# Kernel optimization log

Measured on AMD Instinct MI355X. Metric: run time of the kernel, lower is better.

Reference implementation:

```python
import jax, jax.numpy as jnp
import numpy as np

N_HEADS = 12


def setup_inputs() -> dict:
    key = jax.random.key(0)
    ks = jax.random.split(key, 5)
    B, T, D = 4, 2048, 768
    std = 1.0 / np.sqrt(D)
    return {
        "x": jax.random.normal(ks[0], (B, T, D), jnp.float32),
        "W_qkv": jax.random.normal(ks[1], (3 * D, D), jnp.float32) * std,
        "b_qkv": jax.random.normal(ks[2], (3 * D,), jnp.float32) * 0.02,
        "W_proj": jax.random.normal(ks[3], (D, D), jnp.float32) * std,
        "b_proj": jax.random.normal(ks[4], (D,), jnp.float32) * 0.02,
    }


def reference(x, W_qkv, b_qkv, W_proj, b_proj):
    # x: [B, T, D]; intended 3D path of the module (dropout = eval-mode identity)
    B, T, D = x.shape
    H = N_HEADS
    Dh = D // H
    scale = Dh ** -0.5
    qkv = x @ W_qkv.T + b_qkv                       # [B, T, 3D]
    qkv = qkv.reshape(B, T, 3, H, Dh)
    q = jnp.transpose(qkv[:, :, 0], (0, 2, 1, 3))    # [B, H, T, Dh]
    k = jnp.transpose(qkv[:, :, 1], (0, 2, 1, 3))
    v = jnp.transpose(qkv[:, :, 2], (0, 2, 1, 3))
    attn = jnp.einsum("bhqd,bhkd->bhqk", q, k) * scale  # [B, H, T, T]
    scores = jax.nn.softmax(attn, axis=-1)
    out = jnp.einsum("bhqk,bhkd->bhqd", scores, v)       # [B, H, T, Dh]
    out = jnp.transpose(out, (0, 2, 1, 3)).reshape(B, T, D)
    return out @ W_proj.T + b_proj
```

## Files before the change

### kernel.cpp

```cpp
#include <hip/hip_runtime.h>
#include <hip/hip_bf16.h>
#include <stdint.h>

typedef __bf16 bf16;
typedef __bf16 bf16x8 __attribute__((ext_vector_type(8)));
typedef __bf16 bf16x4 __attribute__((ext_vector_type(4)));
typedef short  s16x4  __attribute__((ext_vector_type(4)));
typedef short  s16x8  __attribute__((ext_vector_type(8)));
typedef float  f32x4  __attribute__((ext_vector_type(4)));

#define N_B 4
#define N_T 2048
#define N_D 768
#define N_H 12
#define N_DH 64
#define M_TOT (N_B * N_T)

__device__ __forceinline__ void async_copy16(const bf16* g, bf16* l) {
    __builtin_amdgcn_global_load_lds(
        (const __attribute__((address_space(1))) unsigned int*)g,
        (__attribute__((address_space(3))) unsigned int*)l,
        16, 0, 0);
}

__launch_bounds__(256)
__global__ void f2bf3(const float* __restrict__ a, bf16* __restrict__ oa, int na,
                      const float* __restrict__ b, bf16* __restrict__ ob, int nb,
                      const float* __restrict__ c, bf16* __restrict__ oc) {
    int i = (blockIdx.x * 256 + threadIdx.x) * 4;
    const float* src; bf16* dst;
    if (i < na)            { src = a; dst = oa; }
    else if (i < na + nb)  { src = b; dst = ob; i -= na; }
    else                   { src = c; dst = oc; i -= na + nb; }
    const float4 v = *(const float4*)(src + i);
    dst[i]     = (bf16)v.x;
    dst[i + 1] = (bf16)v.y;
    dst[i + 2] = (bf16)v.z;
    dst[i + 3] = (bf16)v.w;
}

#define GEMM_CORE(A_PTR, B_PTR, KDIM)                                          \
    __shared__ bf16 lsA[128 * 32];                                             \
    __shared__ bf16 lsB[128 * 32];                                             \
    const int m0 = blockIdx.x * 128;                                           \
    const int n0 = blockIdx.y * 128;                                           \
    const int t  = threadIdx.x;                                                \
    const int w  = t >> 6, l = t & 63;                                         \
    const int wm = w & 1, wn = w >> 1;                                         \
    const int lr = l & 15, lq = l >> 4;                                        \
    f32x4 acc[4][4] = {};                                                      \
    const bf16* Ab = (A_PTR) + (size_t)(m0 + (t >> 2)) * (KDIM) + (t & 3) * 8; \
    const bf16* Bb = (B_PTR) + (size_t)(n0 + (t >> 2)) * (KDIM) + (t & 3) * 8; \
    bf16* lA = lsA + t * 8;                                                    \
    bf16* lB = lsB + t * 8;                                                    \
    for (int k0 = 0; k0 < (KDIM); k0 += 32) {                                  \
        __syncthreads();                                                       \
        async_copy16(Ab + k0, lA);                                             \
        async_copy16(Ab + (size_t)64 * (KDIM) + k0, lA + 2048);                \
        async_copy16(Bb + k0, lB);                                             \
        async_copy16(Bb + (size_t)64 * (KDIM) + k0, lB + 2048);                \
        __syncthreads();                                                       \
        bf16x8 af[4], bfr[4];                                                  \
        for (int i = 0; i < 4; i++) {                                          \
            af[i]  = *(const bf16x8*)(lsA + (wm * 64 + i * 16 + lr) * 32 + lq * 8); \
            bfr[i] = *(const bf16x8*)(lsB + (wn * 64 + i * 16 + lr) * 32 + lq * 8); \
        }                                                                      \
        for (int i = 0; i < 4; i++)                                            \
            for (int j = 0; j < 4; j++)                                        \
                acc[i][j] = __builtin_amdgcn_mfma_f32_16x16x32_bf16(           \
                    af[i], bfr[j], acc[i][j], 0, 0, 0);                        \
    }

__launch_bounds__(256)
__global__ void gemm_qkv(const bf16* __restrict__ X, const bf16* __restrict__ W,
                         const float* __restrict__ bias,
                         bf16* __restrict__ Q, bf16* __restrict__ K,
                         bf16* __restrict__ Vt) {
    GEMM_CORE(X, W, 768)
    for (int i = 0; i < 4; i++) {
        const int rowb = m0 + wm * 64 + i * 16 + lq * 4;
        const int b_ = rowb >> 11, tt = rowb & 2047;
        for (int j = 0; j < 4; j++) {
            const int col   = n0 + wn * 64 + j * 16 + lr;
            const int which = col / 768;
            const int rem   = col - which * 768;
            const int h     = rem >> 6, d = rem & 63;
            const float bv  = bias[col];
            if (which == 2) {
                const int tile = tt >> 6, kl = tt & 63;
                const int ki = kl >> 4, lqv = (kl >> 2) & 3;
                const int idx = 32 * (ki & 1) + 8 * lqv + 4 * (ki >> 1);
                bf16x4 v4;
                for (int r2 = 0; r2 < 4; r2++) v4[r2] = (bf16)(acc[i][j][r2] + bv);
                *(bf16x4*)(Vt + ((size_t)((b_ * N_H + h) * 64 + d)) * 2048
                           + tile * 64 + idx) = v4;
            } else {
                bf16* dst = (which == 0) ? Q : K;
                const float sc = (which == 0) ? 0.18033688f : 1.0f;
                for (int r2 = 0; r2 < 4; r2++)
                    dst[(size_t)(((b_ * N_H + h) << 11) + tt + r2) * 64 + d] =
                        (bf16)((acc[i][j][r2] + bv) * sc);
            }
        }
    }
}

__launch_bounds__(256)
__global__ void gemm_proj(const bf16* __restrict__ O, const bf16* __restrict__ W,
                          const float* __restrict__ bias, float* __restrict__ out) {
    GEMM_CORE(O, W, 768)
    for (int i = 0; i < 4; i++) {
        const int rowb = m0 + wm * 64 + i * 16 + lq * 4;
        for (int j = 0; j < 4; j++) {
            const int col  = n0 + wn * 64 + j * 16 + lr;
            const float bv = bias[col];
            for (int r = 0; r < 4; r++)
                out[(size_t)(rowb + r) * 768 + col] = acc[i][j][r] + bv;
        }
    }
}

__launch_bounds__(256, 3)
__global__ void attn(const bf16* __restrict__ Q, const bf16* __restrict__ K,
                     const bf16* __restrict__ Vt, bf16* __restrict__ O) {
    __shared__ bf16 lsK[2][64 * 64];
    __shared__ bf16 lsV[2][64 * 64];
    const int bid = blockIdx.x;
    const int xcd = bid & 7, slot = bid >> 3;
    const int bh  = xcd + 8 * (slot >> 4);
    const int qt  = slot & 15;
    const int t = threadIdx.x, w = t >> 6, l = t & 63;
    const int lr = l & 15, lq = l >> 4;
    const bf16* Qh  = Q  + (size_t)bh * N_T * 64;
    const bf16* Kh  = K  + (size_t)bh * N_T * 64;
    const bf16* Vth = Vt + (size_t)bh * 64 * N_T;
    const int q0 = qt * 128 + w * 32;

    bf16x8 qf[2][2];
    #pragma unroll
    for (int qg = 0; qg < 2; qg++)
        #pragma unroll
        for (int ks = 0; ks < 2; ks++)
            qf[qg][ks] = *(const bf16x8*)(Qh + (size_t)(q0 + qg * 16 + lr) * 64
                                          + ks * 32 + lq * 8);

    f32x4 oacc[2][4] = {};
    f32x4 lacc[2]    = {};
    const bf16x8 ones8 = {(bf16)1.f, (bf16)1.f, (bf16)1.f, (bf16)1.f,
                          (bf16)1.f, (bf16)1.f, (bf16)1.f, (bf16)1.f};

    #pragma unroll
    for (int j = 0; j < 2; j++) {
        const int u   = t + j * 256;
        const int row = u >> 3;
        const int scn = (u & 7) ^ (row & 7);
        async_copy16(Kh  + (size_t)row * 64 + scn * 8,   lsK[0] + u * 8);
        async_copy16(Vth + (size_t)row * 2048 + scn * 8, lsV[0] + u * 8);
    }

    for (int kt = 0; kt < 32; kt++) {
        const int cur = kt & 1;
        __syncthreads();

        if (kt < 31) {
            #pragma unroll
            for (int j = 0; j < 2; j++) {
                const int u   = t + j * 256;
                const int row = u >> 3;
                const int scn = (u & 7) ^ (row & 7);
                async_copy16(Kh + (size_t)((kt + 1) * 64 + row) * 64 + scn * 8,
                             lsK[cur ^ 1] + u * 8);
                async_copy16(Vth + (size_t)row * 2048 + (kt + 1) * 64 + scn * 8,
                             lsV[cur ^ 1] + u * 8);
            }
        }

        bf16x8 kf[2][4];
        #pragma unroll
        for (int ks = 0; ks < 2; ks++)
            #pragma unroll
            for (int ki = 0; ki < 4; ki++) {
                const int row = ki * 16 + lr;
                kf[ks][ki] = *(const bf16x8*)(lsK[cur] + row * 64
                                              + ((ks * 4 + lq) ^ (lr & 7)) * 8);
            }

        bf16x8 pbf[2][2];
        #pragma unroll
        for (int qg = 0; qg < 2; qg++) {
            f32x4 sacc[4] = {};
            __builtin_amdgcn_s_setprio(1);
            #pragma unroll
            for (int ks = 0; ks < 2; ks++)
                #pragma unroll
                for (int ki = 0; ki < 4; ki++)
                    sacc[ki] = __builtin_amdgcn_mfma_f32_16x16x32_bf16(
                        kf[ks][ki], qf[qg][ks], sacc[ki], 0, 0, 0);
            __builtin_amdgcn_s_setprio(0);
            #pragma unroll
            for (int ks = 0; ks < 2; ks++) {
                bf16x8 pb;
                #pragma unroll
                for (int r = 0; r < 4; r++) {
                    pb[r]     = (bf16)exp2f(sacc[ks][r]);
                    pb[4 + r] = (bf16)exp2f(sacc[ks + 2][r]);
                }
                pbf[qg][ks] = pb;
            }
        }

        __builtin_amdgcn_s_setprio(1);
        #pragma unroll
        for (int ks = 0; ks < 2; ks++)
            #pragma unroll
            for (int dj = 0; dj < 4; dj++) {
                const int row  = dj * 16 + lr;
                const int unit = (4 * ks + lq) ^ (lr & 7);
                bf16x8 vf = *(const bf16x8*)(lsV[cur] + row * 64 + unit * 8);
                #pragma unroll
                for (int qg = 0; qg < 2; qg++)
                    oacc[qg][dj] = __builtin_amdgcn_mfma_f32_16x16x32_bf16(
                        vf, pbf[qg][ks], oacc[qg][dj], 0, 0, 0);
            }
        #pragma unroll
        for (int qg = 0; qg < 2; qg++)
            #pragma unroll
            for (int ks = 0; ks < 2; ks++)
                lacc[qg] = __builtin_amdgcn_mfma_f32_16x16x32_bf16(
                    ones8, pbf[qg][ks], lacc[qg], 0, 0, 0);
        __builtin_amdgcn_s_setprio(0);
    }

    const int b = bh / N_H, h = bh - b * N_H;
    #pragma unroll
    for (int qg = 0; qg < 2; qg++) {
        const float inv_l = 1.0f / lacc[qg][0];
        const int tok = q0 + qg * 16 + lr;
        bf16* Ob = O + ((size_t)b * N_T + tok) * N_D + h * 64;
        #pragma unroll
        for (int dj = 0; dj < 4; dj++) {
            bf16x4 o4;
            #pragma unroll
            for (int r = 0; r < 4; r++) o4[r] = (bf16)(oacc[qg][dj][r] * inv_l);
            *(bf16x4*)(Ob + dj * 16 + lq * 4) = o4;
        }
    }
}

extern "C" void kernel_launch(void* const* d_in, const int* in_sizes, int n_in,
                              void* d_out, int out_size, void* d_ws, size_t ws_size,
                              hipStream_t stream) {
    const float* x      = (const float*)d_in[0];
    const float* W_qkv  = (const float*)d_in[1];
    const float* b_qkv  = (const float*)d_in[2];
    const float* W_proj = (const float*)d_in[3];
    const float* b_proj = (const float*)d_in[4];
    float* out = (float*)d_out;

    char* ws = (char*)d_ws;
    const size_t n_x  = (size_t)M_TOT * N_D;
    const size_t n_wq = (size_t)3 * N_D * N_D;
    const size_t n_wp = (size_t)N_D * N_D;
    const size_t sz_qkv = (size_t)N_B * N_H * N_T * N_DH * sizeof(bf16);

    bf16* xb  = (bf16*)(ws);                 ws += n_x * sizeof(bf16);
    bf16* Wqb = (bf16*)(ws);                 ws += n_wq * sizeof(bf16);
    bf16* Wpb = (bf16*)(ws);                 ws += n_wp * sizeof(bf16);
    bf16* Qb  = (bf16*)(ws);                 ws += sz_qkv;
    bf16* Kb  = (bf16*)(ws);                 ws += sz_qkv;
    bf16* Vtb = (bf16*)(ws);                 ws += sz_qkv;
    bf16* Ob  = (bf16*)(ws);

    dim3 blk(256);
    f2bf3<<<dim3((int)((n_x + n_wq + n_wp) / 1024)), blk, 0, stream>>>(
        x, xb, (int)n_x, W_qkv, Wqb, (int)n_wq, W_proj, Wpb);

    gemm_qkv<<<dim3(M_TOT / 128, 2304 / 128), blk, 0, stream>>>(xb, Wqb, b_qkv, Qb, Kb, Vtb);
    attn<<<dim3(768), dim3(256), 0, stream>>>(Qb, Kb, Vtb, Ob);
    gemm_proj<<<dim3(M_TOT / 128, 768 / 128), blk, 0, stream>>>(Ob, Wpb, b_proj, out);
}
```

Measured before the change: 222.1 us.

## Double-buffer GEMM LDS tiles and narrow projection GEMM tile to 64 columns

The shared GEMM core now uses two LDS buffers per operand. The next K-slice is loaded asynchronously into the idle buffer while the MFMAs run on the current one, which removes one barrier per iteration and overlaps global loads with compute. The output projection GEMM also switches to a 128x64 tile, doubling its block count so more CUs are busy on this small-N GEMM. The cost is double the LDS footprint per block and smaller per-block reuse for the projection.

```diff
diff --git a/kernel.cpp b/kernel.cpp
--- a/kernel.cpp
+++ b/kernel.cpp
@@ -39,34 +39,40 @@
     dst[i + 3] = (bf16)v.w;
 }
 
-#define GEMM_CORE(A_PTR, B_PTR, KDIM)                                          \
-    __shared__ bf16 lsA[128 * 32];                                             \
-    __shared__ bf16 lsB[128 * 32];                                             \
+#define GEMM_STAGE(P, K0)                                                      \
+    async_copy16(Ab + (K0), &lsA[P][t * 8]);                                   \
+    async_copy16(Ab + (size_t)64 * KD + (K0), &lsA[P][2048 + t * 8]);          \
+    async_copy16(Bb + (K0), &lsB[P][t * 8]);                                   \
+    if (TN == 128) async_copy16(Bb + (size_t)64 * KD + (K0), &lsB[P][2048 + t * 8]);
+
+#define GEMM_CORE(A_PTR, B_PTR, KDIM, TN_)                                     \
+    constexpr int KD = (KDIM);                                                 \
+    constexpr int TN = (TN_);                                                  \
+    constexpr int JJ = TN / 32;                                                \
+    constexpr int NT = KD / 32;                                                \
+    __shared__ bf16 lsA[2][128 * 32];                                          \
+    __shared__ bf16 lsB[2][TN * 32];                                           \
     const int m0 = blockIdx.x * 128;                                           \
-    const int n0 = blockIdx.y * 128;                                           \
+    const int n0 = blockIdx.y * TN;                                            \
     const int t  = threadIdx.x;                                                \
     const int w  = t >> 6, l = t & 63;                                         \
     const int wm = w & 1, wn = w >> 1;                                         \
     const int lr = l & 15, lq = l >> 4;                                        \
-    f32x4 acc[4][4] = {};                                                      \
-    const bf16* Ab = (A_PTR) + (size_t)(m0 + (t >> 2)) * (KDIM) + (t & 3) * 8; \
-    const bf16* Bb = (B_PTR) + (size_t)(n0 + (t >> 2)) * (KDIM) + (t & 3) * 8; \
-    bf16* lA = lsA + t * 8;                                                    \
-    bf16* lB = lsB + t * 8;                                                    \
-    for (int k0 = 0; k0 < (KDIM); k0 += 32) {                                  \
+    f32x4 acc[4][JJ] = {};                                                     \
+    const bf16* Ab = (A_PTR) + (size_t)(m0 + (t >> 2)) * KD + (t & 3) * 8;     \
+    const bf16* Bb = (B_PTR) + (size_t)(n0 + (t >> 2)) * KD + (t & 3) * 8;     \
+    GEMM_STAGE(0, 0)                                                           \
+    for (int t0 = 0; t0 < NT; t0++) {                                          \
+        const int p = t0 & 1;                                                  \
         __syncthreads();                                                       \
-        async_copy16(Ab + k0, lA);                                             \
-        async_copy16(Ab + (size_t)64 * (KDIM) + k0, lA + 2048);                \
-        async_copy16(Bb + k0, lB);                                             \
-        async_copy16(Bb + (size_t)64 * (KDIM) + k0, lB + 2048);                \
-        __syncthreads();                                                       \
-        bf16x8 af[4], bfr[4];                                                  \
-        for (int i = 0; i < 4; i++) {                                          \
-            af[i]  = *(const bf16x8*)(lsA + (wm * 64 + i * 16 + lr) * 32 + lq * 8); \
-            bfr[i] = *(const bf16x8*)(lsB + (wn * 64 + i * 16 + lr) * 32 + lq * 8); \
-        }                                                                      \
+        if (t0 + 1 < NT) { GEMM_STAGE(p ^ 1, (t0 + 1) * 32) }                  \
+        bf16x8 af[4], bfr[JJ];                                                 \
         for (int i = 0; i < 4; i++)                                            \
-            for (int j = 0; j < 4; j++)                                        \
+            af[i] = *(const bf16x8*)(&lsA[p][(wm * 64 + i * 16 + lr) * 32 + lq * 8]); \
+        for (int j = 0; j < JJ; j++)                                           \
+            bfr[j] = *(const bf16x8*)(&lsB[p][(wn * (TN / 2) + j * 16 + lr) * 32 + lq * 8]); \
+        for (int i = 0; i < 4; i++)                                            \
+            for (int j = 0; j < JJ; j++)                                       \
                 acc[i][j] = __builtin_amdgcn_mfma_f32_16x16x32_bf16(           \
                     af[i], bfr[j], acc[i][j], 0, 0, 0);                        \
     }
@@ -76,7 +82,7 @@
                          const float* __restrict__ bias,
                          bf16* __restrict__ Q, bf16* __restrict__ K,
                          bf16* __restrict__ Vt) {
-    GEMM_CORE(X, W, 768)
+    GEMM_CORE(X, W, 768, 128)
     for (int i = 0; i < 4; i++) {
         const int rowb = m0 + wm * 64 + i * 16 + lq * 4;
         const int b_ = rowb >> 11, tt = rowb & 2047;
@@ -108,11 +114,11 @@
 __launch_bounds__(256)
 __global__ void gemm_proj(const bf16* __restrict__ O, const bf16* __restrict__ W,
                           const float* __restrict__ bias, float* __restrict__ out) {
-    GEMM_CORE(O, W, 768)
+    GEMM_CORE(O, W, 768, 64)
     for (int i = 0; i < 4; i++) {
         const int rowb = m0 + wm * 64 + i * 16 + lq * 4;
-        for (int j = 0; j < 4; j++) {
-            const int col  = n0 + wn * 64 + j * 16 + lr;
+        for (int j = 0; j < JJ; j++) {
+            const int col  = n0 + wn * (TN / 2) + j * 16 + lr;
             const float bv = bias[col];
             for (int r = 0; r < 4; r++)
                 out[(size_t)(rowb + r) * 768 + col] = acc[i][j][r] + bv;
@@ -277,5 +283,5 @@
 
     gemm_qkv<<<dim3(M_TOT / 128, 2304 / 128), blk, 0, stream>>>(xb, Wqb, b_qkv, Qb, Kb, Vtb);
     attn<<<dim3(768), dim3(256), 0, stream>>>(Qb, Kb, Vtb, Ob);
-    gemm_proj<<<dim3(M_TOT / 128, 768 / 128), blk, 0, stream>>>(Ob, Wpb, b_proj, out);
-}
+    gemm_proj<<<dim3(M_TOT / 128, 768 / 64), blk, 0, stream>>>(Ob, Wpb, b_proj, out);
+}
```

Measured after the change: 229.3 us. 3.2% more time.
